# Kernel optimization log

Measured on AMD Instinct MI355X. Metric: run time of the kernel, lower is better.

## Reference

```python
import jax, jax.numpy as jnp
import numpy as np

B, S, D = 4, 1024, 1024
H, HD = 16, 64  # num_heads, head_dim; H*HD == D (qkv_features)
NEG_BIG = -1e10


def setup_inputs() -> dict:
    key = jax.random.key(0)
    ks = jax.random.split(key, 16)
    inp = {
        'inputs_q': jax.random.normal(ks[0], (B, S, D), jnp.float32),
        'inputs_kv': jax.random.normal(ks[1], (B, S, D), jnp.float32),
        'pos_emb_q': jax.random.normal(ks[2], (B, S, D), jnp.float32),
        'pos_emb_k': jax.random.normal(ks[3], (B, S, D), jnp.float32),
        'pos_emb_v': jax.random.normal(ks[4], (B, S, D), jnp.float32),
        'key_padding_mask': jnp.ones((B, S), jnp.float32),
    }
    scale = 1.0 / np.sqrt(D)
    inp['wq'] = jax.random.normal(ks[5], (D, H, HD), jnp.float32) * scale
    inp['bq'] = jnp.zeros((H, HD), jnp.float32)
    inp['wk'] = jax.random.normal(ks[6], (D, H, HD), jnp.float32) * scale
    inp['bk'] = jnp.zeros((H, HD), jnp.float32)
    inp['wv'] = jax.random.normal(ks[7], (D, H, HD), jnp.float32) * scale
    inp['bv'] = jnp.zeros((H, HD), jnp.float32)
    inp['wo'] = jax.random.normal(ks[8], (H, HD, D), jnp.float32) * scale
    inp['bo'] = jnp.zeros((D,), jnp.float32)
    return inp


def reference(inputs_q, inputs_kv, pos_emb_q, pos_emb_k, pos_emb_v,
              key_padding_mask, wq, bq, wk, bk, wv, bv, wo, bo):
    # Add positional embeddings before QKV projections (DETR style).
    q_in = inputs_q + pos_emb_q
    k_in = inputs_kv + pos_emb_k
    v_in = inputs_kv + pos_emb_v
    # DenseGeneral: [b,s,f] x [f,h,d] -> [b,s,h,d]
    q = jnp.einsum('bsf,fhd->bshd', q_in, wq) + bq
    k = jnp.einsum('bsf,fhd->bshd', k_in, wk) + bk
    v = jnp.einsum('bsf,fhd->bshd', v_in, wv) + bv
    # Additive key-padding bias, broadcast to [b,1,1,kv].
    bias = ((1.0 - key_padding_mask) * NEG_BIG)[:, None, None, :]
    q = q / jnp.sqrt(jnp.asarray(HD, q.dtype))
    attn = jnp.einsum('bqhd,bkhd->bhqk', q, k) + bias
    attn = jax.nn.softmax(attn, axis=-1)
    # (train=False: no dropout; identity capture layer is a no-op.)
    x = jnp.einsum('bhqk,bkhd->bqhd', attn, v)
    # Output projection over (heads, head_dim).
    out = jnp.einsum('bqhd,hdf->bqf', x, wo) + bo
    return out
```

## Files before the change

kernel.cpp:

```cpp
#include <hip/hip_runtime.h>
#include <hip/hip_bf16.h>
#include <stdint.h>

typedef __bf16 bf16_t;
typedef __bf16 bf16x8 __attribute__((ext_vector_type(8)));
typedef __bf16 bf16x4v __attribute__((ext_vector_type(4)));
typedef float  f32x4  __attribute__((ext_vector_type(4)));
typedef float  f32x16 __attribute__((ext_vector_type(16)));
typedef unsigned int u32;
typedef u32 u32x4 __attribute__((ext_vector_type(4)));

#define NEG_BIG (-1e10f)

__device__ __forceinline__ void load_lds16(const void* gsrc, void* ldst) {
  __builtin_amdgcn_global_load_lds(
      (__attribute__((address_space(1))) void*)(gsrc),
      (__attribute__((address_space(3))) void*)(ldst), 16, 0, 0);
}

__device__ __forceinline__ u32 cvt_pk_bf16(float lo, float hi) {
  u32 r;
  asm("v_cvt_pk_bf16_f32 %0, %1, %2" : "=v"(r) : "v"(lo), "v"(hi));
  return r;
}

__global__ __launch_bounds__(256) void k_prep(
    const float4* __restrict__ iq, const float4* __restrict__ ikv,
    const float4* __restrict__ pq, const float4* __restrict__ pk,
    const float4* __restrict__ pv,
    bf16_t* __restrict__ Xq, bf16_t* __restrict__ Xk, bf16_t* __restrict__ Xv)
{
  int i = blockIdx.x * 256 + threadIdx.x;
  float4 a = iq[i], b = ikv[i];
  float4 eq = pq[i], ek = pk[i], ev = pv[i];
  bf16x4v q, k, v;
  q[0] = (bf16_t)(a.x + eq.x); q[1] = (bf16_t)(a.y + eq.y);
  q[2] = (bf16_t)(a.z + eq.z); q[3] = (bf16_t)(a.w + eq.w);
  k[0] = (bf16_t)(b.x + ek.x); k[1] = (bf16_t)(b.y + ek.y);
  k[2] = (bf16_t)(b.z + ek.z); k[3] = (bf16_t)(b.w + ek.w);
  v[0] = (bf16_t)(b.x + ev.x); v[1] = (bf16_t)(b.y + ev.y);
  v[2] = (bf16_t)(b.z + ev.z); v[3] = (bf16_t)(b.w + ev.w);
  *(bf16x4v*)&Xq[(size_t)i*4] = q;
  *(bf16x4v*)&Xk[(size_t)i*4] = k;
  *(bf16x4v*)&Xv[(size_t)i*4] = v;
}

__global__ __launch_bounds__(256) void k_wtrans(
    const float* __restrict__ wq, const float* __restrict__ wk,
    const float* __restrict__ wv, const float* __restrict__ wo,
    bf16_t* __restrict__ Wqt, bf16_t* __restrict__ Wkt,
    bf16_t* __restrict__ Wvt, bf16_t* __restrict__ Wot)
{
  __shared__ float t[64][65];
  int z = blockIdx.z;
  const float* src = z==0 ? wq : z==1 ? wk : z==2 ? wv : wo;
  bf16_t*      dst = z==0 ? Wqt : z==1 ? Wkt : z==2 ? Wvt : Wot;
  int n0 = blockIdx.x * 64, k0 = blockIdx.y * 64;
  int c = threadIdx.x & 63, rb = threadIdx.x >> 6;
  #pragma unroll
  for (int i = 0; i < 16; ++i) {
    int r = i*4 + rb;
    t[r][c] = src[(size_t)(k0 + r)*1024 + n0 + c];
  }
  __syncthreads();
  #pragma unroll
  for (int i = 0; i < 16; ++i) {
    int r = i*4 + rb;
    dst[(size_t)(n0 + r)*1024 + k0 + c] = (bf16_t)t[c][r];
  }
}

__global__ __launch_bounds__(256, 2) void k_gemm_qkv(
    const bf16_t* __restrict__ Xq, const bf16_t* __restrict__ Xk, const bf16_t* __restrict__ Xv,
    const bf16_t* __restrict__ Wqt, const bf16_t* __restrict__ Wkt, const bf16_t* __restrict__ Wvt,
    const float* __restrict__ bq, const float* __restrict__ bk, const float* __restrict__ bv,
    bf16_t* __restrict__ Qo, bf16_t* __restrict__ Ko, bf16_t* __restrict__ Vo)
{
  const int L = blockIdx.x + (blockIdx.y << 3) + (blockIdx.z << 8);
  const int w = (L & 7) * 96 + (L >> 3);
  const int bx = w & 7, by = (w >> 3) & 31, bz = w >> 8;

  const bf16_t* A  = bz==0 ? Xq : bz==1 ? Xk : Xv;
  const bf16_t* Bt = bz==0 ? Wqt : bz==1 ? Wkt : Wvt;
  const float* bias = bz==0 ? bq : bz==1 ? bk : bv;
  bf16_t* C = bz==0 ? Qo : bz==1 ? Ko : Vo;
  const float scale = (bz==0) ? 0.125f : 1.0f;

  __shared__ bf16_t As[2][128*64];
  __shared__ bf16_t Bs[2][128*64];

  const int tid = threadIdx.x, lane = tid & 63, wid = tid >> 6;
  const int wm = wid >> 1, wn = wid & 1;
  const int bm0 = by * 128, bn0 = bx * 128;
  const int g = lane >> 4, c = lane & 15;

  f32x4 acc[4][4] = {};
  const int sr  = lane >> 3;
  const int sch = lane & 7;

  #define STAGE(bufi, kt_)                                                       \
    { _Pragma("unroll")                                                          \
      for (int i = 0; i < 4; ++i) {                                              \
        int r  = wid*32 + i*8 + sr;                                              \
        int ca = sch ^ (r & 7);                                                  \
        load_lds16(A  + (size_t)(bm0 + r)*1024 + (size_t)(kt_)*64 + ca*8,        \
                   &As[bufi][(wid*32 + i*8)*64]);                                \
        load_lds16(Bt + (size_t)(bn0 + r)*1024 + (size_t)(kt_)*64 + ca*8,        \
                   &Bs[bufi][(wid*32 + i*8)*64]);                                \
      } }

  STAGE(0, 0);
  __syncthreads();

  for (int kt = 0; kt < 16; ++kt) {
    const int buf = kt & 1;
    if (kt < 15) STAGE(buf ^ 1, kt + 1);

    #pragma unroll
    for (int kk = 0; kk < 2; ++kk) {
      bf16x8 af[4], bfr[4];
      #pragma unroll
      for (int m = 0; m < 4; ++m) {
        int row = wm*64 + m*16 + c;
        int ch  = (kk*4 + g) ^ (row & 7);
        af[m] = *(const bf16x8*)&As[buf][row*64 + ch*8];
      }
      #pragma unroll
      for (int n = 0; n < 4; ++n) {
        int row = wn*64 + n*16 + c;
        int ch  = (kk*4 + g) ^ (row & 7);
        bfr[n] = *(const bf16x8*)&Bs[buf][row*64 + ch*8];
      }
      #pragma unroll
      for (int m = 0; m < 4; ++m)
        #pragma unroll
        for (int n = 0; n < 4; ++n)
          acc[m][n] = __builtin_amdgcn_mfma_f32_16x16x32_bf16(af[m], bfr[n], acc[m][n], 0, 0, 0);
    }
    if (kt < 15) __syncthreads();
  }

  #pragma unroll
  for (int n = 0; n < 4; ++n) {
    int col = bn0 + wn*64 + n*16 + c;
    float bn_ = bias[col];
    #pragma unroll
    for (int m = 0; m < 4; ++m) {
      int row0 = bm0 + wm*64 + m*16 + g*4;
      #pragma unroll
      for (int r = 0; r < 4; ++r) {
        float v = (acc[m][n][r] + bn_) * scale;
        C[(size_t)(row0 + r)*1024 + col] = (bf16_t)v;
      }
    }
  }
  #undef STAGE
}

__global__ __launch_bounds__(256) void k_vtrans(
    const bf16_t* __restrict__ V, bf16_t* __restrict__ Vt)
{
  __shared__ uint32_t t[64][65];
  int bh = blockIdx.y;
  int s0 = blockIdx.x * 64;
  int b = bh >> 4, h = bh & 15;
  int c = threadIdx.x & 63, rb = threadIdx.x >> 6;
  const uint16_t* src = (const uint16_t*)V + (size_t)(b*1024 + s0)*1024 + h*64;
  #pragma unroll
  for (int i = 0; i < 16; ++i) {
    int r = i*4 + rb;
    t[r][c] = src[(size_t)r*1024 + c];
  }
  __syncthreads();
  uint16_t* dst = (uint16_t*)Vt + (size_t)(bh*64)*1024 + s0;
  #pragma unroll
  for (int i = 0; i < 16; ++i) {
    int r = i*4 + rb;
    dst[(size_t)r*1024 + c] = (uint16_t)t[c][r];
  }
}

__global__ __launch_bounds__(256, 2) void k_attn2(
    const bf16_t* __restrict__ Qm, const bf16_t* __restrict__ Km,
    const bf16_t* __restrict__ Vt, const float* __restrict__ mask,
    bf16_t* __restrict__ X2)
{
  __shared__ bf16_t Ks[2][64*64];
  __shared__ bf16_t Vs[2][64*64];
  __shared__ float  bias_lds[1024];
  __shared__ float  l_lds[4][32];

  const int qt = blockIdx.x, h = blockIdx.y, b = blockIdx.z;
  const int tid = threadIdx.x, lane = tid & 63, wid = tid >> 6;
  const int lq = lane & 31;
  const int hi = lane >> 5;

  {
    float4 m4 = *(const float4*)&mask[b*1024 + tid*4];
    float4 b4;
    b4.x = (1.0f - m4.x) * NEG_BIG;
    b4.y = (1.0f - m4.y) * NEG_BIG;
    b4.z = (1.0f - m4.z) * NEG_BIG;
    b4.w = (1.0f - m4.w) * NEG_BIG;
    *(float4*)&bias_lds[tid*4] = b4;
  }

  const int q0w = qt*128 + wid*32;
  bf16x8 qf[4];
  #pragma unroll
  for (int kb = 0; kb < 4; ++kb)
    qf[kb] = *(const bf16x8*)&Qm[(size_t)(b*1024 + q0w + lq)*1024 + h*64 + kb*16 + hi*8];

  f32x16 oacc[2] = {};
  float mrow = -1e30f, lsum = 0.f;

  const int sr8 = (lane >> 3);
  const int sc8 = lane & 7;
  #define STAGE(bufi, kv0)                                                        \
    {                                                                             \
      _Pragma("unroll")                                                           \
      for (int cc = 0; cc < 2; ++cc) {                                            \
        int r  = cc*32 + wid*8 + sr8;                                             \
        int ca = sc8 ^ (r & 7);                                                   \
        load_lds16(Km + (size_t)(b*1024 + (kv0) + r)*1024 + h*64 + ca*8,          \
                   &Ks[bufi][(cc*32 + wid*8)*64]);                                \
        load_lds16(Vt + (size_t)((b*16 + h)*64 + r)*1024 + (kv0) + ca*8,          \
                   &Vs[bufi][(cc*32 + wid*8)*64]);                                \
      }                                                                           \
    }

  STAGE(0, 0);
  __syncthreads();

  for (int kt = 0; kt < 16; ++kt) {
    const int buf = kt & 1;
    if (kt < 15) STAGE(buf ^ 1, (kt + 1) * 64);

    f32x16 s[2];
    #pragma unroll
    for (int blk = 0; blk < 2; ++blk) {
      f32x16 acc = {};
      #pragma unroll
      for (int kb = 0; kb < 4; ++kb) {
        int row = blk*32 + lq;
        int ch  = (kb*2 + hi) ^ (row & 7);
        bf16x8 kf = *(const bf16x8*)&Ks[buf][row*64 + ch*8];
        acc = __builtin_amdgcn_mfma_f32_32x32x16_bf16(kf, qf[kb], acc, 0, 0, 0);
      }
      s[blk] = acc;
    }

    #pragma unroll
    for (int blk = 0; blk < 2; ++blk)
      #pragma unroll
      for (int g2 = 0; g2 < 4; ++g2) {
        float4 b4 = *(const float4*)&bias_lds[kt*64 + blk*32 + g2*8 + hi*4];
        s[blk][g2*4+0] += b4.x;
        s[blk][g2*4+1] += b4.y;
        s[blk][g2*4+2] += b4.z;
        s[blk][g2*4+3] += b4.w;
      }

    float pmax = s[0][0];
    #pragma unroll
    for (int blk = 0; blk < 2; ++blk)
      #pragma unroll
      for (int r = 0; r < 16; ++r) pmax = fmaxf(pmax, s[blk][r]);
    pmax = fmaxf(pmax, __shfl_xor(pmax, 32, 64));

    if (!__all(pmax - mrow <= 8.0f)) {
      float mnew = fmaxf(mrow, pmax);
      float sc = __expf(mrow - mnew);
      lsum *= sc;
      #pragma unroll
      for (int nb = 0; nb < 2; ++nb)
        #pragma unroll
        for (int i = 0; i < 16; ++i) oacc[nb][i] *= sc;
      mrow = mnew;
    }

    float rs = 0.f;
    #pragma unroll
    for (int blk = 0; blk < 2; ++blk)
      #pragma unroll
      for (int r = 0; r < 16; ++r) {
        float p = __expf(s[blk][r] - mrow);
        s[blk][r] = p;
        rs += p;
      }
    lsum += rs + __shfl_xor(rs, 32, 64);

    u32 paw[4][4];
    #pragma unroll
    for (int blk = 0; blk < 2; ++blk)
      #pragma unroll
      for (int half = 0; half < 2; ++half) {
        int base = half * 8;
        #pragma unroll
        for (int w2 = 0; w2 < 2; ++w2) {
          u32 x = cvt_pk_bf16(s[blk][base + 2*w2],     s[blk][base + 2*w2 + 1]);
          u32 y = cvt_pk_bf16(s[blk][base + 4 + 2*w2], s[blk][base + 4 + 2*w2 + 1]);
          asm("v_permlane32_swap_b32 %0, %1" : "+v"(x), "+v"(y));
          paw[blk*2 + half][w2]     = x;
          paw[blk*2 + half][w2 + 2] = y;
        }
      }

    #pragma unroll
    for (int ks = 0; ks < 4; ++ks) {
      u32x4 t = { paw[ks][0], paw[ks][1], paw[ks][2], paw[ks][3] };
      bf16x8 pa = __builtin_bit_cast(bf16x8, t);
      #pragma unroll
      for (int nb = 0; nb < 2; ++nb) {
        int row = nb*32 + lq;
        int ch  = (ks*2 + hi) ^ (row & 7);
        bf16x8 vf = *(const bf16x8*)&Vs[buf][row*64 + ch*8];
        oacc[nb] = __builtin_amdgcn_mfma_f32_32x32x16_bf16(pa, vf, oacc[nb], 0, 0, 0);
      }
    }
    __syncthreads();
  }

  l_lds[wid][lq] = lsum;
  __syncthreads();
  #pragma unroll
  for (int g2 = 0; g2 < 4; ++g2)
    #pragma unroll
    for (int j = 0; j < 4; ++j) {
      int reg  = g2*4 + j;
      int qrow = j + 8*g2 + 4*hi;
      float inv = 1.0f / l_lds[wid][qrow];
      #pragma unroll
      for (int nb = 0; nb < 2; ++nb)
        X2[(size_t)(b*1024 + q0w + qrow)*1024 + h*64 + nb*32 + lq] =
            (bf16_t)(oacc[nb][reg] * inv);
    }
  #undef STAGE
}

__global__ __launch_bounds__(256, 2) void k_gemm_out(
    const bf16_t* __restrict__ A, const bf16_t* __restrict__ Bt,
    const float* __restrict__ bo, float* __restrict__ C)
{
  const int L = blockIdx.x + (blockIdx.y << 3);
  const int w = (L & 7) * 32 + (L >> 3);
  const int bx = w & 7, by = w >> 3;

  __shared__ bf16_t As[2][128*64];
  __shared__ bf16_t Bs[2][128*64];

  const int tid = threadIdx.x, lane = tid & 63, wid = tid >> 6;
  const int wm = wid >> 1, wn = wid & 1;
  const int bm0 = by * 128, bn0 = bx * 128;
  const int g = lane >> 4, c = lane & 15;

  f32x4 acc[4][4] = {};
  const int sr  = lane >> 3;
  const int sch = lane & 7;

  #define STAGEO(bufi, kt_)                                                      \
    { _Pragma("unroll")                                                          \
      for (int i = 0; i < 4; ++i) {                                              \
        int r  = wid*32 + i*8 + sr;                                              \
        int ca = sch ^ (r & 7);                                                  \
        load_lds16(A  + (size_t)(bm0 + r)*1024 + (size_t)(kt_)*64 + ca*8,        \
                   &As[bufi][(wid*32 + i*8)*64]);                                \
        load_lds16(Bt + (size_t)(bn0 + r)*1024 + (size_t)(kt_)*64 + ca*8,        \
                   &Bs[bufi][(wid*32 + i*8)*64]);                                \
      } }

  STAGEO(0, 0);
  __syncthreads();

  for (int kt = 0; kt < 16; ++kt) {
    const int buf = kt & 1;
    if (kt < 15) STAGEO(buf ^ 1, kt + 1);

    #pragma unroll
    for (int kk = 0; kk < 2; ++kk) {
      bf16x8 af[4], bfr[4];
      #pragma unroll
      for (int m = 0; m < 4; ++m) {
        int row = wm*64 + m*16 + c;
        int ch  = (kk*4 + g) ^ (row & 7);
        af[m] = *(const bf16x8*)&As[buf][row*64 + ch*8];
      }
      #pragma unroll
      for (int n = 0; n < 4; ++n) {
        int row = wn*64 + n*16 + c;
        int ch  = (kk*4 + g) ^ (row & 7);
        bfr[n] = *(const bf16x8*)&Bs[buf][row*64 + ch*8];
      }
      #pragma unroll
      for (int m = 0; m < 4; ++m)
        #pragma unroll
        for (int n = 0; n < 4; ++n)
          acc[m][n] = __builtin_amdgcn_mfma_f32_16x16x32_bf16(af[m], bfr[n], acc[m][n], 0, 0, 0);
    }
    if (kt < 15) __syncthreads();
  }

  #pragma unroll
  for (int n = 0; n < 4; ++n) {
    int col = bn0 + wn*64 + n*16 + c;
    float bn_ = bo[col];
    #pragma unroll
    for (int m = 0; m < 4; ++m) {
      int row0 = bm0 + wm*64 + m*16 + g*4;
      #pragma unroll
      for (int r = 0; r < 4; ++r)
        C[(size_t)(row0 + r)*1024 + col] = acc[m][n][r] + bn_;
    }
  }
  #undef STAGEO
}

extern "C" void kernel_launch(void* const* d_in, const int* in_sizes, int n_in,
                              void* d_out, int out_size, void* d_ws, size_t ws_size,
                              hipStream_t stream) {
  const float* iq   = (const float*)d_in[0];
  const float* ikv  = (const float*)d_in[1];
  const float* pq   = (const float*)d_in[2];
  const float* pk   = (const float*)d_in[3];
  const float* pv   = (const float*)d_in[4];
  const float* mask = (const float*)d_in[5];
  const float* wq   = (const float*)d_in[6];
  const float* bq   = (const float*)d_in[7];
  const float* wk   = (const float*)d_in[8];
  const float* bk   = (const float*)d_in[9];
  const float* wv   = (const float*)d_in[10];
  const float* bv   = (const float*)d_in[11];
  const float* wo   = (const float*)d_in[12];
  const float* bo   = (const float*)d_in[13];
  float* out = (float*)d_out;

  char* ws = (char*)d_ws;
  bf16_t* Xq  = (bf16_t*)(ws + (size_t)( 0u<<20));
  bf16_t* Xk  = (bf16_t*)(ws + (size_t)( 8u<<20));
  bf16_t* Xv  = (bf16_t*)(ws + (size_t)(16u<<20));
  bf16_t* Wqt = (bf16_t*)(ws + (size_t)(24u<<20));
  bf16_t* Wkt = (bf16_t*)(ws + (size_t)(26u<<20));
  bf16_t* Wvt = (bf16_t*)(ws + (size_t)(28u<<20));
  bf16_t* Wot = (bf16_t*)(ws + (size_t)(30u<<20));
  bf16_t* Q   = (bf16_t*)(ws + (size_t)(32u<<20));
  bf16_t* K   = (bf16_t*)(ws + (size_t)(40u<<20));
  bf16_t* V   = (bf16_t*)(ws + (size_t)(48u<<20));
  bf16_t* Vt  = (bf16_t*)(ws + (size_t)(56u<<20));
  bf16_t* X2  = (bf16_t*)(ws + (size_t)(64u<<20));

  k_prep<<<4096, 256, 0, stream>>>((const float4*)iq, (const float4*)ikv,
      (const float4*)pq, (const float4*)pk, (const float4*)pv, Xq, Xk, Xv);
  k_wtrans<<<dim3(16,16,4), 256, 0, stream>>>(wq, wk, wv, wo, Wqt, Wkt, Wvt, Wot);
  k_gemm_qkv<<<dim3(8,32,3), 256, 0, stream>>>(Xq, Xk, Xv, Wqt, Wkt, Wvt,
                                               bq, bk, bv, Q, K, V);
  k_vtrans<<<dim3(16,64), 256, 0, stream>>>(V, Vt);
  k_attn2<<<dim3(8,16,4), 256, 0, stream>>>(Q, K, Vt, mask, X2);
  k_gemm_out<<<dim3(8,32), 256, 0, stream>>>(X2, Wot, bo, out);
}
```

Before: 122.0 us.

## Merge prep kernels, fuse V transpose into QKV GEMM, restructure GEMM pipelining

The activation-prep and weight-transpose kernels are merged into a single launch, and the separate V-transpose kernel is removed. The QKV GEMM now writes V directly in transposed per-head layout from its epilogue. Both GEMMs change their LDS double-buffering to prefetch two stages ahead, with explicit vmcnt waits, raw s_barrier calls and s_setprio around the MFMA block. The goal is to cut launch count, avoid an extra round trip of V through memory, and overlap loads better, at the cost of scattered 8-byte stores in the V epilogue.

```diff
diff --git a/kernel.cpp b/kernel.cpp
--- a/kernel.cpp
+++ b/kernel.cpp
@@ -24,98 +24,97 @@
   return r;
 }
 
-__global__ __launch_bounds__(256) void k_prep(
-    const float4* __restrict__ iq, const float4* __restrict__ ikv,
-    const float4* __restrict__ pq, const float4* __restrict__ pk,
-    const float4* __restrict__ pv,
-    bf16_t* __restrict__ Xq, bf16_t* __restrict__ Xk, bf16_t* __restrict__ Xv)
-{
-  int i = blockIdx.x * 256 + threadIdx.x;
-  float4 a = iq[i], b = ikv[i];
-  float4 eq = pq[i], ek = pk[i], ev = pv[i];
-  bf16x4v q, k, v;
-  q[0] = (bf16_t)(a.x + eq.x); q[1] = (bf16_t)(a.y + eq.y);
-  q[2] = (bf16_t)(a.z + eq.z); q[3] = (bf16_t)(a.w + eq.w);
-  k[0] = (bf16_t)(b.x + ek.x); k[1] = (bf16_t)(b.y + ek.y);
-  k[2] = (bf16_t)(b.z + ek.z); k[3] = (bf16_t)(b.w + ek.w);
-  v[0] = (bf16_t)(b.x + ev.x); v[1] = (bf16_t)(b.y + ev.y);
-  v[2] = (bf16_t)(b.z + ev.z); v[3] = (bf16_t)(b.w + ev.w);
-  *(bf16x4v*)&Xq[(size_t)i*4] = q;
-  *(bf16x4v*)&Xk[(size_t)i*4] = k;
-  *(bf16x4v*)&Xv[(size_t)i*4] = v;
-}
-
-__global__ __launch_bounds__(256) void k_wtrans(
+__global__ __launch_bounds__(256) void k_prep_w(
+    const float* __restrict__ iq, const float* __restrict__ ikv,
+    const float* __restrict__ pq, const float* __restrict__ pk, const float* __restrict__ pv,
     const float* __restrict__ wq, const float* __restrict__ wk,
     const float* __restrict__ wv, const float* __restrict__ wo,
-    bf16_t* __restrict__ Wqt, bf16_t* __restrict__ Wkt,
-    bf16_t* __restrict__ Wvt, bf16_t* __restrict__ Wot)
+    bf16_t* __restrict__ Xq, bf16_t* __restrict__ Xk, bf16_t* __restrict__ Xv,
+    bf16_t* __restrict__ Wt, bf16_t* __restrict__ Wot)
 {
   __shared__ float t[64][65];
-  int z = blockIdx.z;
-  const float* src = z==0 ? wq : z==1 ? wk : z==2 ? wv : wo;
-  bf16_t*      dst = z==0 ? Wqt : z==1 ? Wkt : z==2 ? Wvt : Wot;
-  int n0 = blockIdx.x * 64, k0 = blockIdx.y * 64;
-  int c = threadIdx.x & 63, rb = threadIdx.x >> 6;
-  #pragma unroll
-  for (int i = 0; i < 16; ++i) {
-    int r = i*4 + rb;
-    t[r][c] = src[(size_t)(k0 + r)*1024 + n0 + c];
-  }
-  __syncthreads();
-  #pragma unroll
-  for (int i = 0; i < 16; ++i) {
-    int r = i*4 + rb;
-    dst[(size_t)(n0 + r)*1024 + k0 + c] = (bf16_t)t[c][r];
+  if (blockIdx.x < 4096) {
+    int i = blockIdx.x * 256 + threadIdx.x;
+    float4 a = ((const float4*)iq)[i], b = ((const float4*)ikv)[i];
+    float4 eq = ((const float4*)pq)[i], ek = ((const float4*)pk)[i], ev = ((const float4*)pv)[i];
+    bf16x4v q, k, v;
+    q[0] = (bf16_t)(a.x + eq.x); q[1] = (bf16_t)(a.y + eq.y);
+    q[2] = (bf16_t)(a.z + eq.z); q[3] = (bf16_t)(a.w + eq.w);
+    k[0] = (bf16_t)(b.x + ek.x); k[1] = (bf16_t)(b.y + ek.y);
+    k[2] = (bf16_t)(b.z + ek.z); k[3] = (bf16_t)(b.w + ek.w);
+    v[0] = (bf16_t)(b.x + ev.x); v[1] = (bf16_t)(b.y + ev.y);
+    v[2] = (bf16_t)(b.z + ev.z); v[3] = (bf16_t)(b.w + ev.w);
+    *(bf16x4v*)&Xq[(size_t)i*4] = q;
+    *(bf16x4v*)&Xk[(size_t)i*4] = k;
+    *(bf16x4v*)&Xv[(size_t)i*4] = v;
+  } else {
+    int bid = blockIdx.x - 4096;
+    int z = bid >> 8, rem = bid & 255;
+    const float* src = z==0 ? wq : z==1 ? wk : z==2 ? wv : wo;
+    bf16_t*      dst = z < 3 ? (Wt + (size_t)z*(1u<<20)) : Wot;
+    int n0 = (rem & 15) << 6, k0 = (rem >> 4) << 6;
+    int c = threadIdx.x & 63, rb = threadIdx.x >> 6;
+    #pragma unroll
+    for (int i = 0; i < 16; ++i) {
+      int r = i*4 + rb;
+      t[r][c] = src[(size_t)(k0 + r)*1024 + n0 + c];
+    }
+    __syncthreads();
+    #pragma unroll
+    for (int i = 0; i < 16; ++i) {
+      int r = i*4 + rb;
+      dst[(size_t)(n0 + r)*1024 + k0 + c] = (bf16_t)t[c][r];
+    }
   }
 }
 
 __global__ __launch_bounds__(256, 2) void k_gemm_qkv(
     const bf16_t* __restrict__ Xq, const bf16_t* __restrict__ Xk, const bf16_t* __restrict__ Xv,
-    const bf16_t* __restrict__ Wqt, const bf16_t* __restrict__ Wkt, const bf16_t* __restrict__ Wvt,
+    const bf16_t* __restrict__ Wt,
     const float* __restrict__ bq, const float* __restrict__ bk, const float* __restrict__ bv,
-    bf16_t* __restrict__ Qo, bf16_t* __restrict__ Ko, bf16_t* __restrict__ Vo)
+    bf16_t* __restrict__ Qo, bf16_t* __restrict__ Ko, bf16_t* __restrict__ Vt)
 {
-  const int L = blockIdx.x + (blockIdx.y << 3) + (blockIdx.z << 8);
+  const int L = blockIdx.x;
   const int w = (L & 7) * 96 + (L >> 3);
-  const int bx = w & 7, by = (w >> 3) & 31, bz = w >> 8;
-
-  const bf16_t* A  = bz==0 ? Xq : bz==1 ? Xk : Xv;
-  const bf16_t* Bt = bz==0 ? Wqt : bz==1 ? Wkt : Wvt;
-  const float* bias = bz==0 ? bq : bz==1 ? bk : bv;
-  bf16_t* C = bz==0 ? Qo : bz==1 ? Ko : Vo;
-  const float scale = (bz==0) ? 0.125f : 1.0f;
+  const int bn = w >> 5, by = w & 31;
+  const int z = bn >> 3;
+  const bf16_t* A = z==0 ? Xq : z==1 ? Xk : Xv;
+  const float* bias = z==0 ? bq : z==1 ? bk : bv;
 
   __shared__ bf16_t As[2][128*64];
   __shared__ bf16_t Bs[2][128*64];
 
   const int tid = threadIdx.x, lane = tid & 63, wid = tid >> 6;
   const int wm = wid >> 1, wn = wid & 1;
-  const int bm0 = by * 128, bn0 = bx * 128;
+  const int bm0 = by * 128;
+  const int bn0g = bn * 128;
   const int g = lane >> 4, c = lane & 15;
+  const int sr = lane >> 3, sch = lane & 7;
 
   f32x4 acc[4][4] = {};
-  const int sr  = lane >> 3;
-  const int sch = lane & 7;
 
   #define STAGE(bufi, kt_)                                                       \
     { _Pragma("unroll")                                                          \
       for (int i = 0; i < 4; ++i) {                                              \
         int r  = wid*32 + i*8 + sr;                                              \
         int ca = sch ^ (r & 7);                                                  \
-        load_lds16(A  + (size_t)(bm0 + r)*1024 + (size_t)(kt_)*64 + ca*8,        \
+        load_lds16(A  + (size_t)(bm0  + r)*1024 + (size_t)(kt_)*64 + ca*8,       \
                    &As[bufi][(wid*32 + i*8)*64]);                                \
-        load_lds16(Bt + (size_t)(bn0 + r)*1024 + (size_t)(kt_)*64 + ca*8,        \
+        load_lds16(Wt + (size_t)(bn0g + r)*1024 + (size_t)(kt_)*64 + ca*8,       \
                    &Bs[bufi][(wid*32 + i*8)*64]);                                \
       } }
 
   STAGE(0, 0);
-  __syncthreads();
+  STAGE(1, 1);
+  asm volatile("s_waitcnt vmcnt(8)" ::: "memory");
+  __builtin_amdgcn_sched_barrier(0);
+  __builtin_amdgcn_s_barrier();
+  __builtin_amdgcn_sched_barrier(0);
 
   for (int kt = 0; kt < 16; ++kt) {
     const int buf = kt & 1;
-    if (kt < 15) STAGE(buf ^ 1, kt + 1);
-
+
+    __builtin_amdgcn_s_setprio(1);
     #pragma unroll
     for (int kk = 0; kk < 2; ++kk) {
       bf16x8 af[4], bfr[4];
@@ -137,46 +136,56 @@
         for (int n = 0; n < 4; ++n)
           acc[m][n] = __builtin_amdgcn_mfma_f32_16x16x32_bf16(af[m], bfr[n], acc[m][n], 0, 0, 0);
     }
-    if (kt < 15) __syncthreads();
-  }
-
-  #pragma unroll
-  for (int n = 0; n < 4; ++n) {
-    int col = bn0 + wn*64 + n*16 + c;
-    float bn_ = bias[col];
-    #pragma unroll
-    for (int m = 0; m < 4; ++m) {
-      int row0 = bm0 + wm*64 + m*16 + g*4;
-      #pragma unroll
-      for (int r = 0; r < 4; ++r) {
-        float v = (acc[m][n][r] + bn_) * scale;
-        C[(size_t)(row0 + r)*1024 + col] = (bf16_t)v;
-      }
+    __builtin_amdgcn_s_setprio(0);
+
+    if (kt < 15) {
+      __builtin_amdgcn_sched_barrier(0);
+      __builtin_amdgcn_s_barrier();
+      __builtin_amdgcn_sched_barrier(0);
+      if (kt < 14) {
+        STAGE(buf, kt + 2);
+        asm volatile("s_waitcnt vmcnt(8)" ::: "memory");
+      } else {
+        asm volatile("s_waitcnt vmcnt(0)" ::: "memory");
+      }
+      __builtin_amdgcn_sched_barrier(0);
+      __builtin_amdgcn_s_barrier();
+      __builtin_amdgcn_sched_barrier(0);
     }
   }
   #undef STAGE
-}
-
-__global__ __launch_bounds__(256) void k_vtrans(
-    const bf16_t* __restrict__ V, bf16_t* __restrict__ Vt)
-{
-  __shared__ uint32_t t[64][65];
-  int bh = blockIdx.y;
-  int s0 = blockIdx.x * 64;
-  int b = bh >> 4, h = bh & 15;
-  int c = threadIdx.x & 63, rb = threadIdx.x >> 6;
-  const uint16_t* src = (const uint16_t*)V + (size_t)(b*1024 + s0)*1024 + h*64;
-  #pragma unroll
-  for (int i = 0; i < 16; ++i) {
-    int r = i*4 + rb;
-    t[r][c] = src[(size_t)r*1024 + c];
-  }
-  __syncthreads();
-  uint16_t* dst = (uint16_t*)Vt + (size_t)(bh*64)*1024 + s0;
-  #pragma unroll
-  for (int i = 0; i < 16; ++i) {
-    int r = i*4 + rb;
-    dst[(size_t)r*1024 + c] = (uint16_t)t[c][r];
+
+  if (z < 2) {
+    bf16_t* C = z==0 ? Qo : Ko;
+    const float scale = z==0 ? 0.125f : 1.0f;
+    #pragma unroll
+    for (int n = 0; n < 4; ++n) {
+      int col = (bn0g & 1023) + wn*64 + n*16 + c;
+      float bn_ = bias[col];
+      #pragma unroll
+      for (int m = 0; m < 4; ++m) {
+        int row0 = bm0 + wm*64 + m*16 + g*4;
+        #pragma unroll
+        for (int r = 0; r < 4; ++r)
+          C[(size_t)(row0 + r)*1024 + col] = (bf16_t)((acc[m][n][r] + bn_) * scale);
+      }
+    }
+  } else {
+    #pragma unroll
+    for (int n = 0; n < 4; ++n) {
+      int colz = (bn0g & 1023) + wn*64 + n*16 + c;
+      float bn_ = bias[colz];
+      int h = colz >> 6, hd = colz & 63;
+      #pragma unroll
+      for (int m = 0; m < 4; ++m) {
+        int row0 = bm0 + wm*64 + m*16 + g*4;
+        int b = row0 >> 10, s0 = row0 & 1023;
+        bf16x4v v4;
+        #pragma unroll
+        for (int r = 0; r < 4; ++r) v4[r] = (bf16_t)(acc[m][n][r] + bn_);
+        *(bf16x4v*)&Vt[(size_t)((b*16 + h)*64 + hd)*1024 + s0] = v4;
+      }
+    }
   }
 }
 
@@ -342,21 +351,20 @@
     const bf16_t* __restrict__ A, const bf16_t* __restrict__ Bt,
     const float* __restrict__ bo, float* __restrict__ C)
 {
-  const int L = blockIdx.x + (blockIdx.y << 3);
+  const int L = blockIdx.x;
   const int w = (L & 7) * 32 + (L >> 3);
-  const int bx = w & 7, by = w >> 3;
+  const int bn = w >> 5, by = w & 31;
 
   __shared__ bf16_t As[2][128*64];
   __shared__ bf16_t Bs[2][128*64];
 
   const int tid = threadIdx.x, lane = tid & 63, wid = tid >> 6;
   const int wm = wid >> 1, wn = wid & 1;
-  const int bm0 = by * 128, bn0 = bx * 128;
+  const int bm0 = by * 128, bn0 = bn * 128;
   const int g = lane >> 4, c = lane & 15;
+  const int sr = lane >> 3, sch = lane & 7;
 
   f32x4 acc[4][4] = {};
-  const int sr  = lane >> 3;
-  const int sch = lane & 7;
 
   #define STAGEO(bufi, kt_)                                                      \
     { _Pragma("unroll")                                                          \
@@ -370,12 +378,16 @@
       } }
 
   STAGEO(0, 0);
-  __syncthreads();
+  STAGEO(1, 1);
+  asm volatile("s_waitcnt vmcnt(8)" ::: "memory");
+  __builtin_amdgcn_sched_barrier(0);
+  __builtin_amdgcn_s_barrier();
+  __builtin_amdgcn_sched_barrier(0);
 
   for (int kt = 0; kt < 16; ++kt) {
     const int buf = kt & 1;
-    if (kt < 15) STAGEO(buf ^ 1, kt + 1);
-
+
+    __builtin_amdgcn_s_setprio(1);
     #pragma unroll
     for (int kk = 0; kk < 2; ++kk) {
       bf16x8 af[4], bfr[4];
@@ -397,8 +409,24 @@
         for (int n = 0; n < 4; ++n)
           acc[m][n] = __builtin_amdgcn_mfma_f32_16x16x32_bf16(af[m], bfr[n], acc[m][n], 0, 0, 0);
     }
-    if (kt < 15) __syncthreads();
-  }
+    __builtin_amdgcn_s_setprio(0);
+
+    if (kt < 15) {
+      __builtin_amdgcn_sched_barrier(0);
+      __builtin_amdgcn_s_barrier();
+      __builtin_amdgcn_sched_barrier(0);
+      if (kt < 14) {
+        STAGEO(buf, kt + 2);
+        asm volatile("s_waitcnt vmcnt(8)" ::: "memory");
+      } else {
+        asm volatile("s_waitcnt vmcnt(0)" ::: "memory");
+      }
+      __builtin_amdgcn_sched_barrier(0);
+      __builtin_amdgcn_s_barrier();
+      __builtin_amdgcn_sched_barrier(0);
+    }
+  }
+  #undef STAGEO
 
   #pragma unroll
   for (int n = 0; n < 4; ++n) {
@@ -412,7 +440,6 @@
         C[(size_t)(row0 + r)*1024 + col] = acc[m][n][r] + bn_;
     }
   }
-  #undef STAGEO
 }
 
 extern "C" void kernel_launch(void* const* d_in, const int* in_sizes, int n_in,
@@ -438,22 +465,16 @@
   bf16_t* Xq  = (bf16_t*)(ws + (size_t)( 0u<<20));
   bf16_t* Xk  = (bf16_t*)(ws + (size_t)( 8u<<20));
   bf16_t* Xv  = (bf16_t*)(ws + (size_t)(16u<<20));
-  bf16_t* Wqt = (bf16_t*)(ws + (size_t)(24u<<20));
-  bf16_t* Wkt = (bf16_t*)(ws + (size_t)(26u<<20));
-  bf16_t* Wvt = (bf16_t*)(ws + (size_t)(28u<<20));
+  bf16_t* Wt  = (bf16_t*)(ws + (size_t)(24u<<20));
   bf16_t* Wot = (bf16_t*)(ws + (size_t)(30u<<20));
   bf16_t* Q   = (bf16_t*)(ws + (size_t)(32u<<20));
   bf16_t* K   = (bf16_t*)(ws + (size_t)(40u<<20));
-  bf16_t* V   = (bf16_t*)(ws + (size_t)(48u<<20));
   bf16_t* Vt  = (bf16_t*)(ws + (size_t)(56u<<20));
   bf16_t* X2  = (bf16_t*)(ws + (size_t)(64u<<20));
 
-  k_prep<<<4096, 256, 0, stream>>>((const float4*)iq, (const float4*)ikv,
-      (const float4*)pq, (const float4*)pk, (const float4*)pv, Xq, Xk, Xv);
-  k_wtrans<<<dim3(16,16,4), 256, 0, stream>>>(wq, wk, wv, wo, Wqt, Wkt, Wvt, Wot);
-  k_gemm_qkv<<<dim3(8,32,3), 256, 0, stream>>>(Xq, Xk, Xv, Wqt, Wkt, Wvt,
-                                               bq, bk, bv, Q, K, V);
-  k_vtrans<<<dim3(16,64), 256, 0, stream>>>(V, Vt);
+  k_prep_w<<<5120, 256, 0, stream>>>(iq, ikv, pq, pk, pv, wq, wk, wv, wo,
+                                     Xq, Xk, Xv, Wt, Wot);
+  k_gemm_qkv<<<768, 256, 0, stream>>>(Xq, Xk, Xv, Wt, bq, bk, bv, Q, K, Vt);
   k_attn2<<<dim3(8,16,4), 256, 0, stream>>>(Q, K, Vt, mask, X2);
-  k_gemm_out<<<dim3(8,32), 256, 0, stream>>>(X2, Wot, bo, out);
-}
+  k_gemm_out<<<256, 256, 0, stream>>>(X2, Wot, bo, out);
+}
```

Measured after the change: 120.1 us. Within noise of the previous version (-1.6%).
